# Kernel optimization log

Measured on AMD Instinct MI355X. Metric: run time of the kernel, lower is better.

## Reference

```python
import jax, jax.numpy as jnp
import numpy as np

B, H, T, D = 2, 16, 2048, 64


def setup_inputs() -> dict:
    key = jax.random.key(0)
    kq, kk, kv, kvm, khm = jax.random.split(key, 5)
    q = jax.random.normal(kq, (B, H, T, D), dtype=jnp.float32)
    k = jax.random.normal(kk, (B, H, D, T), dtype=jnp.float32)  # pre-transposed, matmul(q, k) -> [B,H,T,T]
    v = jax.random.normal(kv, (B, H, T, D), dtype=jnp.float32)
    f = jnp.asarray(float(np.sqrt(D)), dtype=jnp.float32)  # scale divisor
    vmask = (jax.random.uniform(kvm, (B, T)) < 0.9).astype(jnp.float32)
    hmask = (jax.random.uniform(khm, (B, T)) < 0.9).astype(jnp.float32)
    return {"q": q, "k": k, "v": v, "f": f, "vmask": vmask, "hmask": hmask}


def reference(q, k, v, f, vmask, hmask):
    # scores = q @ k / f  -> [B,H,T,T]
    scores = jnp.matmul(q, k) / f
    # padding mask: vmask indexes columns (key positions), hmask indexes rows (query positions)
    pad = vmask[:, None, None, :] * hmask[:, None, :, None]  # [B,1,T,T], broadcasts over H
    s = scores * pad
    s = jnp.where(s == 0, jnp.asarray(1e-10, s.dtype), s)  # masked_fill(new_scores == 0, 1e-10)
    # causal mask: -inf strictly above diagonal
    t = s.shape[-1]
    causal = jnp.triu(jnp.full((t, t), -jnp.inf, dtype=s.dtype), k=1)
    s = s + causal
    return jnp.matmul(jax.nn.softmax(s, axis=-1), v)  # [B,H,T,D]
```

## Files before the change

### kernel.cpp

```cpp
#include <hip/hip_runtime.h>
#include <hip/hip_bf16.h>

#define B_ 2
#define H_ 16
#define T_ 2048
#define D_ 64
#define BH (B_*H_)

typedef __attribute__((ext_vector_type(8))) short bf16x8;
typedef __attribute__((ext_vector_type(16))) float f32x16;
typedef __attribute__((ext_vector_type(4))) unsigned int u32x4;
typedef unsigned int u32;

typedef __attribute__((address_space(3))) void lds_void;
typedef __attribute__((address_space(1))) const void gbl_void;

__device__ __forceinline__ ushort f2bu(float x){
    __hip_bfloat16 h = __float2bfloat16(x);
    return __builtin_bit_cast(ushort, h);
}
__device__ __forceinline__ u32 cvtpk(float a, float b){
    u32 r; asm("v_cvt_pk_bf16_f32 %0, %1, %2" : "=v"(r) : "v"(a), "v"(b)); return r;
}
__device__ __forceinline__ float xhalf_max(float x){
    float a = x, b = x;
    asm("" : "+v"(b));
    asm("v_permlane32_swap_b32 %0, %1" : "+v"(a), "+v"(b));
    return fmaxf(a, b);
}
__device__ __forceinline__ float xhalf_sum(float x){
    float a = x, b = x;
    asm("" : "+v"(b));
    asm("v_permlane32_swap_b32 %0, %1" : "+v"(a), "+v"(b));
    return a + b;
}

__global__ __launch_bounds__(256) void prep(
    const float* __restrict__ k, const float* __restrict__ v,
    const float* __restrict__ vm,
    ushort* __restrict__ KT, ushort* __restrict__ VT)
{
    __shared__ ushort tl[64][65];
    const int bh = blockIdx.x;
    const bool isK = (blockIdx.y < 32);
    const int ty = isK ? blockIdx.y : (blockIdx.y - 32);
    const int i0 = isK ? 0 : ty*64;
    const int j0 = isK ? ty*64 : 0;
    const int M = isK ? D_ : T_;
    const int N = isK ? T_ : D_;
    const float* s = (isK ? k : v) + (size_t)bh*M*N;
    ushort*      d = (isK ? KT : VT) + (size_t)bh*M*N;
    const int tid = threadIdx.x;
    const int rr = tid>>4, c4 = (tid&15)*4;
    #pragma unroll
    for (int p=0;p<4;++p){
        int a = p*16+rr;
        float4 x = *reinterpret_cast<const float4*>(&s[(size_t)(i0+a)*N + j0 + c4]);
        tl[c4+0][a]=f2bu(x.x); tl[c4+1][a]=f2bu(x.y);
        tl[c4+2][a]=f2bu(x.z); tl[c4+3][a]=f2bu(x.w);
    }
    __syncthreads();
    #pragma unroll
    for (int p=0;p<4;++p){
        int bb = p*16+rr;
        ushort4 u;
        u.x=tl[bb][c4]; u.y=tl[bb][c4+1]; u.z=tl[bb][c4+2]; u.w=tl[bb][c4+3];
        if (isK && vm[(size_t)(bh>>4)*T_ + j0 + bb] == 0.f) { u.x=0;u.y=0;u.z=0;u.w=0; }
        *reinterpret_cast<ushort4*>(&d[(size_t)(j0+bb)*M + i0 + c4]) = u;
    }
}

__global__ __launch_bounds__(64, 2) void attn_fwd(
    const float* __restrict__ q, const float* __restrict__ fp,
    const float* __restrict__ hmask,
    const ushort* __restrict__ KT,
    const ushort* __restrict__ VT,
    float* __restrict__ out)
{
    __shared__ __align__(16) ushort sbuf[8192];

    const int bid = blockIdx.x;
    const int bh = bid & (BH-1);
    const int qw = 63 - (bid >> 5);
    const int i0 = qw*32;
    const int lane = threadIdx.x & 63;
    const int col = lane & 31;
    const int hi  = lane >> 5;

    const ushort* KTb = KT + (size_t)bh*T_*D_;
    const ushort* VTb = VT + (size_t)bh*T_*D_;

    const float hmv = hmask[(size_t)(bh>>4)*T_ + i0 + col];
    const float sscale = 1.4426950408889634f / fp[0];
    const float qs = (hmv != 0.f) ? sscale : 0.f;
    const float NINF = -__builtin_inff();

    const float* qp = q + (size_t)bh*T_*D_ + (size_t)(i0+col)*D_ + hi*8;
    bf16x8 qf[4];
    #pragma unroll
    for (int dc=0; dc<4; ++dc){
        float4 x0 = *reinterpret_cast<const float4*>(qp + dc*16);
        float4 x1 = *reinterpret_cast<const float4*>(qp + dc*16 + 4);
        u32x4 dw;
        dw[0] = cvtpk(x0.x*qs, x0.y*qs);
        dw[1] = cvtpk(x0.z*qs, x0.w*qs);
        dw[2] = cvtpk(x1.x*qs, x1.y*qs);
        dw[3] = cvtpk(x1.z*qs, x1.w*qs);
        qf[dc] = __builtin_bit_cast(bf16x8, dw);
    }

    float m_run = 0.f, l_run = 0.f;
    f32x16 o0, o1;
    #pragma unroll
    for (int r=0;r<16;++r){ o0[r]=0.f; o1[r]=0.f; }

    const unsigned uoff = (unsigned)(lane*16);
    const unsigned swz = ((unsigned)(col&7)) << 4;

    auto stage = [&](int t){
        char* ldsK = (char*)&sbuf[0];
        char* ldsV = (char*)&sbuf[4096];
        const char* kbase = (const char*)KTb + (size_t)t*8192;
        #pragma unroll
        for (int i=0;i<8;++i){
            const unsigned u = i*1024u + uoff;
            const unsigned su = u ^ (((u>>7)&7u)<<4);
            __builtin_amdgcn_global_load_lds(
                (gbl_void*)(kbase + su),
                (lds_void*)(ldsK + i*1024), 16, 0, 0);
        }
        #pragma unroll
        for (int i=0;i<8;++i){
            const unsigned u = i*1024u + uoff;
            const unsigned dR = u>>7;
            const unsigned inr = (u&127u) ^ ((dR&7u)<<4);
            const char* src = (const char*)VTb + (size_t)dR*(T_*2) + (size_t)t*128 + inr;
            __builtin_amdgcn_global_load_lds(
                (gbl_void*)src,
                (lds_void*)(ldsV + i*1024), 16, 0, 0);
        }
    };

    const int n = (qw >> 1) + 1;
    stage(0);
    asm volatile("s_waitcnt vmcnt(0)" ::: "memory");

    for (int t=0; t<n; ++t){
        const int j0 = t*64;

        const char* sKb = (const char*)&sbuf[0];
        bf16x8 kf[8];
        #pragma unroll
        for (int kt=0;kt<2;++kt)
            #pragma unroll
            for (int dc=0;dc<4;++dc)
                kf[kt*4+dc] = *reinterpret_cast<const bf16x8*>(
                    sKb + (((unsigned)(kt*4096 + dc*32 + col*128 + hi*16)) ^ swz));
        const char* sVb = (const char*)&sbuf[4096];
        bf16x8 vf[8];
        #pragma unroll
        for (int f=0;f<8;++f)
            vf[f] = *reinterpret_cast<const bf16x8*>(
                sVb + (((unsigned)((f>>2)*4096 + (f&3)*32 + col*128 + hi*16)) ^ swz));

        asm volatile("s_waitcnt lgkmcnt(0)" ::: "memory");
        __builtin_amdgcn_sched_barrier(0);
        if (t+1 < n) stage(t+1);

        f32x16 s0, s1;
        #pragma unroll
        for (int r=0;r<16;++r){ s0[r]=0.f; s1[r]=0.f; }
        #pragma unroll
        for (int dc=0;dc<4;++dc){
            s0 = __builtin_amdgcn_mfma_f32_32x32x16_bf16(kf[dc],   qf[dc], s0, 0,0,0);
            s1 = __builtin_amdgcn_mfma_f32_32x32x16_bf16(kf[4+dc], qf[dc], s1, 0,0,0);
        }

        if (j0 + 63 > i0) {
            const int th0 = i0 + col - j0 - 4*hi;
            const int th1 = th0 - 32;
            #pragma unroll
            for (int r=0;r<16;++r){
                const int basr = (r&3) + 8*(r>>2);
                s0[r] = (basr <= th0) ? s0[r] : NINF;
                s1[r] = (basr <= th1) ? s1[r] : NINF;
            }
        }

        float tm[8];
        #pragma unroll
        for (int i=0;i<8;++i)
            tm[i] = fmaxf(fmaxf(s0[2*i], s0[2*i+1]), fmaxf(s1[2*i], s1[2*i+1]));
        #pragma unroll
        for (int st=4; st>=1; st>>=1)
            #pragma unroll
            for (int i=0;i<st;++i) tm[i] = fmaxf(tm[i], tm[i+st]);
        const float mt = xhalf_max(tm[0]);
        if (__any(!(mt <= m_run + 8.0f))) {
            const float mn = fmaxf(m_run, mt);
            const float fac = __builtin_amdgcn_exp2f(m_run - mn);
            m_run = mn; l_run *= fac;
            #pragma unroll
            for (int r=0;r<16;++r){ o0[r]*=fac; o1[r]*=fac; }
        }

        float tsum[8];
        #pragma unroll
        for (int i=0;i<8;++i){
            float p00 = __builtin_amdgcn_exp2f(s0[2*i]   - m_run);
            float p01 = __builtin_amdgcn_exp2f(s0[2*i+1] - m_run);
            float p10 = __builtin_amdgcn_exp2f(s1[2*i]   - m_run);
            float p11 = __builtin_amdgcn_exp2f(s1[2*i+1] - m_run);
            s0[2*i]=p00; s0[2*i+1]=p01; s1[2*i]=p10; s1[2*i+1]=p11;
            tsum[i] = (p00+p01) + (p10+p11);
        }
        #pragma unroll
        for (int st=4; st>=1; st>>=1)
            #pragma unroll
            for (int i=0;i<st;++i) tsum[i] += tsum[i+st];
        l_run += xhalf_sum(tsum[0]);

        bf16x8 pb[4];
        #pragma unroll
        for (int c2=0;c2<4;++c2){
            const f32x16& ps = (c2<2) ? s0 : s1;
            const int rb = (c2&1)*8;
            u32 a0 = cvtpk(ps[rb+0], ps[rb+1]);
            u32 a1 = cvtpk(ps[rb+2], ps[rb+3]);
            u32 a2 = cvtpk(ps[rb+4], ps[rb+5]);
            u32 a3 = cvtpk(ps[rb+6], ps[rb+7]);
            asm("v_permlane32_swap_b32 %0, %1" : "+v"(a0), "+v"(a2));
            asm("v_permlane32_swap_b32 %0, %1" : "+v"(a1), "+v"(a3));
            u32x4 dw; dw[0]=a0; dw[1]=a1; dw[2]=a2; dw[3]=a3;
            pb[c2] = __builtin_bit_cast(bf16x8, dw);
        }

        #pragma unroll
        for (int c2=0;c2<4;++c2){
            o0 = __builtin_amdgcn_mfma_f32_32x32x16_bf16(vf[c2],   pb[c2], o0, 0,0,0);
            o1 = __builtin_amdgcn_mfma_f32_32x32x16_bf16(vf[4+c2], pb[c2], o1, 0,0,0);
        }

        asm volatile("s_waitcnt vmcnt(0)" ::: "memory");
    }

    const float rinv = 1.0f / l_run;
    float* op = out + (size_t)bh*T_*D_ + (size_t)(i0+col)*D_;
    #pragma unroll
    for (int q4=0;q4<4;++q4){
        float4 a = {o0[4*q4]*rinv, o0[4*q4+1]*rinv, o0[4*q4+2]*rinv, o0[4*q4+3]*rinv};
        *reinterpret_cast<float4*>(op + 8*q4 + 4*hi) = a;
        float4 b = {o1[4*q4]*rinv, o1[4*q4+1]*rinv, o1[4*q4+2]*rinv, o1[4*q4+3]*rinv};
        *reinterpret_cast<float4*>(op + 32 + 8*q4 + 4*hi) = b;
    }
}

extern "C" void kernel_launch(void* const* d_in, const int* in_sizes, int n_in,
                              void* d_out, int out_size, void* d_ws, size_t ws_size,
                              hipStream_t stream) {
    const float* q  = (const float*)d_in[0];
    const float* k  = (const float*)d_in[1];
    const float* v  = (const float*)d_in[2];
    const float* f  = (const float*)d_in[3];
    const float* vm = (const float*)d_in[4];
    const float* hm = (const float*)d_in[5];
    float* out = (float*)d_out;

    const size_t slab = (size_t)BH * T_ * D_;
    ushort* KT = (ushort*)d_ws;
    ushort* VT = KT + slab;

    hipLaunchKernelGGL(prep, dim3(BH, 64), dim3(256), 0, stream, k, v, vm, KT, VT);

    dim3 grid(2048);
    dim3 block(64);
    hipLaunchKernelGGL(attn_fwd, grid, block, 0, stream, q, f, hm, KT, VT, out);
}
```

Before: 51.51 us.

## Pair causal query tiles per block and split KV range across two waves

Measured after the change: 61.45 us. 1.19x slower.

```diff
diff --git a/kernel.cpp b/kernel.cpp
--- a/kernel.cpp
+++ b/kernel.cpp
@@ -70,56 +70,36 @@
     }
 }
 
-__global__ __launch_bounds__(64, 2) void attn_fwd(
+__global__ __launch_bounds__(128, 2) void attn_fwd(
     const float* __restrict__ q, const float* __restrict__ fp,
     const float* __restrict__ hmask,
     const ushort* __restrict__ KT,
     const ushort* __restrict__ VT,
     float* __restrict__ out)
 {
-    __shared__ __align__(16) ushort sbuf[8192];
+    __shared__ __align__(16) ushort sbuf[2][8192];
 
     const int bid = blockIdx.x;
     const int bh = bid & (BH-1);
-    const int qw = 63 - (bid >> 5);
-    const int i0 = qw*32;
-    const int lane = threadIdx.x & 63;
+    const int a  = bid >> 5;
+    const int tid = threadIdx.x;
+    const int lane = tid & 63;
+    const int wid  = tid >> 6;
     const int col = lane & 31;
     const int hi  = lane >> 5;
 
     const ushort* KTb = KT + (size_t)bh*T_*D_;
     const ushort* VTb = VT + (size_t)bh*T_*D_;
-
-    const float hmv = hmask[(size_t)(bh>>4)*T_ + i0 + col];
     const float sscale = 1.4426950408889634f / fp[0];
-    const float qs = (hmv != 0.f) ? sscale : 0.f;
     const float NINF = -__builtin_inff();
-
-    const float* qp = q + (size_t)bh*T_*D_ + (size_t)(i0+col)*D_ + hi*8;
-    bf16x8 qf[4];
-    #pragma unroll
-    for (int dc=0; dc<4; ++dc){
-        float4 x0 = *reinterpret_cast<const float4*>(qp + dc*16);
-        float4 x1 = *reinterpret_cast<const float4*>(qp + dc*16 + 4);
-        u32x4 dw;
-        dw[0] = cvtpk(x0.x*qs, x0.y*qs);
-        dw[1] = cvtpk(x0.z*qs, x0.w*qs);
-        dw[2] = cvtpk(x1.x*qs, x1.y*qs);
-        dw[3] = cvtpk(x1.z*qs, x1.w*qs);
-        qf[dc] = __builtin_bit_cast(bf16x8, dw);
-    }
-
-    float m_run = 0.f, l_run = 0.f;
-    f32x16 o0, o1;
-    #pragma unroll
-    for (int r=0;r<16;++r){ o0[r]=0.f; o1[r]=0.f; }
 
     const unsigned uoff = (unsigned)(lane*16);
     const unsigned swz = ((unsigned)(col&7)) << 4;
+    char* wbase = (char*)&sbuf[0][0] + wid*16384;
 
     auto stage = [&](int t){
-        char* ldsK = (char*)&sbuf[0];
-        char* ldsV = (char*)&sbuf[4096];
+        char* ldsK = wbase;
+        char* ldsV = wbase + 8192;
         const char* kbase = (const char*)KTb + (size_t)t*8192;
         #pragma unroll
         for (int i=0;i<8;++i){
@@ -141,117 +121,179 @@
         }
     };
 
-    const int n = (qw >> 1) + 1;
-    stage(0);
-    asm volatile("s_waitcnt vmcnt(0)" ::: "memory");
-
-    for (int t=0; t<n; ++t){
-        const int j0 = t*64;
-
-        const char* sKb = (const char*)&sbuf[0];
-        bf16x8 kf[8];
+    #pragma unroll 1
+    for (int phase=0; phase<2; ++phase){
+        const int g = phase ? a : (63 - a);
+        const int i0 = g*32;
+        const int n = (g>>1) + 1;
+        const int h = (n+1) >> 1;
+        const int ts = wid ? h : 0;
+        const int te = wid ? n : h;
+
+        const float hmv = hmask[(size_t)(bh>>4)*T_ + i0 + col];
+        const float qs = (hmv != 0.f) ? sscale : 0.f;
+
+        bf16x8 qf[4];
+        {
+            const float* qp = q + (size_t)bh*T_*D_ + (size_t)(i0+col)*D_ + hi*8;
+            #pragma unroll
+            for (int dc=0; dc<4; ++dc){
+                float4 x0 = *reinterpret_cast<const float4*>(qp + dc*16);
+                float4 x1 = *reinterpret_cast<const float4*>(qp + dc*16 + 4);
+                u32x4 dw;
+                dw[0] = cvtpk(x0.x*qs, x0.y*qs);
+                dw[1] = cvtpk(x0.z*qs, x0.w*qs);
+                dw[2] = cvtpk(x1.x*qs, x1.y*qs);
+                dw[3] = cvtpk(x1.z*qs, x1.w*qs);
+                qf[dc] = __builtin_bit_cast(bf16x8, dw);
+            }
+        }
+
+        float m_run = 0.f, l_run = 0.f;
+        f32x16 o0, o1;
         #pragma unroll
-        for (int kt=0;kt<2;++kt)
+        for (int r=0;r<16;++r){ o0[r]=0.f; o1[r]=0.f; }
+
+        if (ts < te){
+            stage(ts);
+            asm volatile("s_waitcnt vmcnt(0)" ::: "memory");
+
+            for (int t=ts; t<te; ++t){
+                const int j0 = t*64;
+
+                bf16x8 kf[8];
+                #pragma unroll
+                for (int kt=0;kt<2;++kt)
+                    #pragma unroll
+                    for (int dc=0;dc<4;++dc)
+                        kf[kt*4+dc] = *reinterpret_cast<const bf16x8*>(
+                            wbase + (((unsigned)(kt*4096 + dc*32 + col*128 + hi*16)) ^ swz));
+                bf16x8 vf[8];
+                #pragma unroll
+                for (int f=0;f<8;++f)
+                    vf[f] = *reinterpret_cast<const bf16x8*>(
+                        wbase + 8192 + (((unsigned)((f>>2)*4096 + (f&3)*32 + col*128 + hi*16)) ^ swz));
+
+                asm volatile("s_waitcnt lgkmcnt(0)" ::: "memory");
+                __builtin_amdgcn_sched_barrier(0);
+                if (t+1 < te) stage(t+1);
+
+                f32x16 s0, s1;
+                #pragma unroll
+                for (int r=0;r<16;++r){ s0[r]=0.f; s1[r]=0.f; }
+                #pragma unroll
+                for (int dc=0;dc<4;++dc){
+                    s0 = __builtin_amdgcn_mfma_f32_32x32x16_bf16(kf[dc],   qf[dc], s0, 0,0,0);
+                    s1 = __builtin_amdgcn_mfma_f32_32x32x16_bf16(kf[4+dc], qf[dc], s1, 0,0,0);
+                }
+
+                if (j0 + 63 > i0) {
+                    const int th0 = i0 + col - j0 - 4*hi;
+                    const int th1 = th0 - 32;
+                    #pragma unroll
+                    for (int r=0;r<16;++r){
+                        const int basr = (r&3) + 8*(r>>2);
+                        s0[r] = (basr <= th0) ? s0[r] : NINF;
+                        s1[r] = (basr <= th1) ? s1[r] : NINF;
+                    }
+                }
+
+                float tm[8];
+                #pragma unroll
+                for (int i=0;i<8;++i)
+                    tm[i] = fmaxf(fmaxf(s0[2*i], s0[2*i+1]), fmaxf(s1[2*i], s1[2*i+1]));
+                #pragma unroll
+                for (int st=4; st>=1; st>>=1)
+                    #pragma unroll
+                    for (int i=0;i<st;++i) tm[i] = fmaxf(tm[i], tm[i+st]);
+                const float mt = xhalf_max(tm[0]);
+                if (__any(!(mt <= m_run + 8.0f))) {
+                    const float mn = fmaxf(m_run, mt);
+                    const float fac = __builtin_amdgcn_exp2f(m_run - mn);
+                    m_run = mn; l_run *= fac;
+                    #pragma unroll
+                    for (int r=0;r<16;++r){ o0[r]*=fac; o1[r]*=fac; }
+                }
+
+                float tsum[8];
+                #pragma unroll
+                for (int i=0;i<8;++i){
+                    float p00 = __builtin_amdgcn_exp2f(s0[2*i]   - m_run);
+                    float p01 = __builtin_amdgcn_exp2f(s0[2*i+1] - m_run);
+                    float p10 = __builtin_amdgcn_exp2f(s1[2*i]   - m_run);
+                    float p11 = __builtin_amdgcn_exp2f(s1[2*i+1] - m_run);
+                    s0[2*i]=p00; s0[2*i+1]=p01; s1[2*i]=p10; s1[2*i+1]=p11;
+                    tsum[i] = (p00+p01) + (p10+p11);
+                }
+                #pragma unroll
+                for (int st=4; st>=1; st>>=1)
+                    #pragma unroll
+                    for (int i=0;i<st;++i) tsum[i] += tsum[i+st];
+                l_run += xhalf_sum(tsum[0]);
+
+                bf16x8 pb[4];
+                #pragma unroll
+                for (int c2=0;c2<4;++c2){
+                    const f32x16& ps = (c2<2) ? s0 : s1;
+                    const int rb = (c2&1)*8;
+                    u32 a0 = cvtpk(ps[rb+0], ps[rb+1]);
+                    u32 a1 = cvtpk(ps[rb+2], ps[rb+3]);
+                    u32 a2 = cvtpk(ps[rb+4], ps[rb+5]);
+                    u32 a3 = cvtpk(ps[rb+6], ps[rb+7]);
+                    asm("v_permlane32_swap_b32 %0, %1" : "+v"(a0), "+v"(a2));
+                    asm("v_permlane32_swap_b32 %0, %1" : "+v"(a1), "+v"(a3));
+                    u32x4 dw; dw[0]=a0; dw[1]=a1; dw[2]=a2; dw[3]=a3;
+                    pb[c2] = __builtin_bit_cast(bf16x8, dw);
+                }
+
+                #pragma unroll
+                for (int c2=0;c2<4;++c2){
+                    o0 = __builtin_amdgcn_mfma_f32_32x32x16_bf16(vf[c2],   pb[c2], o0, 0,0,0);
+                    o1 = __builtin_amdgcn_mfma_f32_32x32x16_bf16(vf[4+c2], pb[c2], o1, 0,0,0);
+                }
+
+                asm volatile("s_waitcnt vmcnt(0)" ::: "memory");
+            }
+        }
+
+        __syncthreads();
+        float* sl = (float*)&sbuf[1][0] + (size_t)lane*36;
+        if (wid == 1){
             #pragma unroll
-            for (int dc=0;dc<4;++dc)
-                kf[kt*4+dc] = *reinterpret_cast<const bf16x8*>(
-                    sKb + (((unsigned)(kt*4096 + dc*32 + col*128 + hi*16)) ^ swz));
-        const char* sVb = (const char*)&sbuf[4096];
-        bf16x8 vf[8];
-        #pragma unroll
-        for (int f=0;f<8;++f)
-            vf[f] = *reinterpret_cast<const bf16x8*>(
-                sVb + (((unsigned)((f>>2)*4096 + (f&3)*32 + col*128 + hi*16)) ^ swz));
-
-        asm volatile("s_waitcnt lgkmcnt(0)" ::: "memory");
-        __builtin_amdgcn_sched_barrier(0);
-        if (t+1 < n) stage(t+1);
-
-        f32x16 s0, s1;
-        #pragma unroll
-        for (int r=0;r<16;++r){ s0[r]=0.f; s1[r]=0.f; }
-        #pragma unroll
-        for (int dc=0;dc<4;++dc){
-            s0 = __builtin_amdgcn_mfma_f32_32x32x16_bf16(kf[dc],   qf[dc], s0, 0,0,0);
-            s1 = __builtin_amdgcn_mfma_f32_32x32x16_bf16(kf[4+dc], qf[dc], s1, 0,0,0);
-        }
-
-        if (j0 + 63 > i0) {
-            const int th0 = i0 + col - j0 - 4*hi;
-            const int th1 = th0 - 32;
+            for (int q4=0;q4<4;++q4){
+                *reinterpret_cast<float4*>(sl + 4*q4)      =
+                    (float4){o0[4*q4],o0[4*q4+1],o0[4*q4+2],o0[4*q4+3]};
+                *reinterpret_cast<float4*>(sl + 16 + 4*q4) =
+                    (float4){o1[4*q4],o1[4*q4+1],o1[4*q4+2],o1[4*q4+3]};
+            }
+            sl[32] = m_run; sl[33] = l_run;
+        }
+        __syncthreads();
+        if (wid == 0){
+            const float m1 = sl[32], l1 = sl[33];
+            const float M = fmaxf(m_run, m1);
+            const float e0 = __builtin_amdgcn_exp2f(m_run - M);
+            const float e1 = __builtin_amdgcn_exp2f(m1 - M);
+            const float L = l_run*e0 + l1*e1;
+            const float rinv = 1.0f / L;
+            float* op = out + (size_t)bh*T_*D_ + (size_t)(i0+col)*D_;
             #pragma unroll
-            for (int r=0;r<16;++r){
-                const int basr = (r&3) + 8*(r>>2);
-                s0[r] = (basr <= th0) ? s0[r] : NINF;
-                s1[r] = (basr <= th1) ? s1[r] : NINF;
+            for (int q4=0;q4<4;++q4){
+                float4 pa = *reinterpret_cast<const float4*>(sl + 4*q4);
+                float4 ra = {(o0[4*q4]*e0   + pa.x*e1)*rinv,
+                             (o0[4*q4+1]*e0 + pa.y*e1)*rinv,
+                             (o0[4*q4+2]*e0 + pa.z*e1)*rinv,
+                             (o0[4*q4+3]*e0 + pa.w*e1)*rinv};
+                *reinterpret_cast<float4*>(op + 8*q4 + 4*hi) = ra;
+                float4 pb4 = *reinterpret_cast<const float4*>(sl + 16 + 4*q4);
+                float4 rb = {(o1[4*q4]*e0   + pb4.x*e1)*rinv,
+                             (o1[4*q4+1]*e0 + pb4.y*e1)*rinv,
+                             (o1[4*q4+2]*e0 + pb4.z*e1)*rinv,
+                             (o1[4*q4+3]*e0 + pb4.w*e1)*rinv};
+                *reinterpret_cast<float4*>(op + 32 + 8*q4 + 4*hi) = rb;
             }
         }
-
-        float tm[8];
-        #pragma unroll
-        for (int i=0;i<8;++i)
-            tm[i] = fmaxf(fmaxf(s0[2*i], s0[2*i+1]), fmaxf(s1[2*i], s1[2*i+1]));
-        #pragma unroll
-        for (int st=4; st>=1; st>>=1)
-            #pragma unroll
-            for (int i=0;i<st;++i) tm[i] = fmaxf(tm[i], tm[i+st]);
-        const float mt = xhalf_max(tm[0]);
-        if (__any(!(mt <= m_run + 8.0f))) {
-            const float mn = fmaxf(m_run, mt);
-            const float fac = __builtin_amdgcn_exp2f(m_run - mn);
-            m_run = mn; l_run *= fac;
-            #pragma unroll
-            for (int r=0;r<16;++r){ o0[r]*=fac; o1[r]*=fac; }
-        }
-
-        float tsum[8];
-        #pragma unroll
-        for (int i=0;i<8;++i){
-            float p00 = __builtin_amdgcn_exp2f(s0[2*i]   - m_run);
-            float p01 = __builtin_amdgcn_exp2f(s0[2*i+1] - m_run);
-            float p10 = __builtin_amdgcn_exp2f(s1[2*i]   - m_run);
-            float p11 = __builtin_amdgcn_exp2f(s1[2*i+1] - m_run);
-            s0[2*i]=p00; s0[2*i+1]=p01; s1[2*i]=p10; s1[2*i+1]=p11;
-            tsum[i] = (p00+p01) + (p10+p11);
-        }
-        #pragma unroll
-        for (int st=4; st>=1; st>>=1)
-            #pragma unroll
-            for (int i=0;i<st;++i) tsum[i] += tsum[i+st];
-        l_run += xhalf_sum(tsum[0]);
-
-        bf16x8 pb[4];
-        #pragma unroll
-        for (int c2=0;c2<4;++c2){
-            const f32x16& ps = (c2<2) ? s0 : s1;
-            const int rb = (c2&1)*8;
-            u32 a0 = cvtpk(ps[rb+0], ps[rb+1]);
-            u32 a1 = cvtpk(ps[rb+2], ps[rb+3]);
-            u32 a2 = cvtpk(ps[rb+4], ps[rb+5]);
-            u32 a3 = cvtpk(ps[rb+6], ps[rb+7]);
-            asm("v_permlane32_swap_b32 %0, %1" : "+v"(a0), "+v"(a2));
-            asm("v_permlane32_swap_b32 %0, %1" : "+v"(a1), "+v"(a3));
-            u32x4 dw; dw[0]=a0; dw[1]=a1; dw[2]=a2; dw[3]=a3;
-            pb[c2] = __builtin_bit_cast(bf16x8, dw);
-        }
-
-        #pragma unroll
-        for (int c2=0;c2<4;++c2){
-            o0 = __builtin_amdgcn_mfma_f32_32x32x16_bf16(vf[c2],   pb[c2], o0, 0,0,0);
-            o1 = __builtin_amdgcn_mfma_f32_32x32x16_bf16(vf[4+c2], pb[c2], o1, 0,0,0);
-        }
-
-        asm volatile("s_waitcnt vmcnt(0)" ::: "memory");
-    }
-
-    const float rinv = 1.0f / l_run;
-    float* op = out + (size_t)bh*T_*D_ + (size_t)(i0+col)*D_;
-    #pragma unroll
-    for (int q4=0;q4<4;++q4){
-        float4 a = {o0[4*q4]*rinv, o0[4*q4+1]*rinv, o0[4*q4+2]*rinv, o0[4*q4+3]*rinv};
-        *reinterpret_cast<float4*>(op + 8*q4 + 4*hi) = a;
-        float4 b = {o1[4*q4]*rinv, o1[4*q4+1]*rinv, o1[4*q4+2]*rinv, o1[4*q4+3]*rinv};
-        *reinterpret_cast<float4*>(op + 32 + 8*q4 + 4*hi) = b;
+        __syncthreads();
     }
 }
 
@@ -272,7 +314,7 @@
 
     hipLaunchKernelGGL(prep, dim3(BH, 64), dim3(256), 0, stream, k, v, vm, KT, VT);
 
-    dim3 grid(2048);
-    dim3 block(64);
+    dim3 grid(1024);
+    dim3 block(128);
     hipLaunchKernelGGL(attn_fwd, grid, block, 0, stream, q, f, hm, KT, VT, out);
 }
```
